# Kernel tuning notes

Measured on AMD Instinct MI355X. Metric: run time of the kernel, lower is better.

Reference implementation:

```python
import jax, jax.numpy as jnp
import numpy as np

WINDOW_SIZE = 11
SIGMA = 1.5
COLOR_TRANS = np.array([65.738, 129.057, 25.064], dtype=np.float32)
C1 = (0.01 * 255) ** 2
C2 = (0.03 * 255) ** 2


def _make_window(ws=WINDOW_SIZE, sigma=SIGMA):
    x = np.arange(ws, dtype=np.float32)
    g = np.exp(-((x - ws // 2) ** 2) / (2.0 * sigma ** 2))
    g = g / g.sum()
    w2d = np.outer(g, g).astype(np.float32)  # [ws, ws]
    return jnp.asarray(w2d[None, None])      # [1,1,ws,ws] OIHW


def _conv(x, w):
    # x: [B,1,H,W], w: [1,1,ws,ws], VALID padding, single channel
    return jax.lax.conv_general_dilated(
        x, w, window_strides=(1, 1), padding='VALID',
        dimension_numbers=('NCHW', 'OIHW', 'NCHW'))


def _luma(img):
    # img: [B,H,W,>=3] in [-1,1] -> [B,1,H,W] luma in [16,235]-ish
    rgb = (img[..., :3] + 1.0) / 2.0 * 255.0
    y = jnp.matmul(rgb, jnp.asarray(COLOR_TRANS)) / 256.0 + 16.0
    return y[:, None, :, :]


def setup_inputs() -> dict:
    key = jax.random.key(0)
    k1, k2 = jax.random.split(key)
    shape = (32, 512, 512, 3)
    img1 = jax.random.uniform(k1, shape, jnp.float32, -1.0, 1.0)
    img2 = jax.random.uniform(k2, shape, jnp.float32, -1.0, 1.0)
    return {"img1": img1, "img2": img2}


def reference(img1, img2):
    w = _make_window()
    x1 = _luma(img1)
    x2 = _luma(img2)
    mu1 = _conv(x1, w)
    mu2 = _conv(x2, w)
    mu1_sq = mu1 * mu1
    mu2_sq = mu2 * mu2
    mu1_mu2 = mu1 * mu2
    sigma1_sq = _conv(x1 * x1, w) - mu1_sq
    sigma2_sq = _conv(x2 * x2, w) - mu2_sq
    sigma12 = _conv(x1 * x2, w) - mu1_mu2
    ssim_map = ((2 * mu1_mu2 + C1) * (2 * sigma12 + C2)) / (
        (mu1_sq + mu2_sq + C1) * (sigma1_sq + sigma2_sq + C2))
    return jnp.mean(ssim_map)
```

## Files before the change

### kernel.cpp

```cpp
#include <hip/hip_runtime.h>
#include <math.h>

#define BATCH 32
#define H 512
#define W 512
#define OUTD 502
#define WS 11
#define STRIP 32
#define INROWS 42
#define WPAD 80

#define C1F 6.5025f
#define C2F 58.5225f
#define N_OUT_TOTAL 8064128.0

struct GW { float g[WS]; };

__device__ __forceinline__ float luma3(float r, float g, float b) {
    r = (r + 1.f) * 127.5f; g = (g + 1.f) * 127.5f; b = (b + 1.f) * 127.5f;
    return (r * 65.738f + g * 129.057f + b * 25.064f) * (1.f / 256.f) + 16.f;
}

__global__ __launch_bounds__(256) void ssim_stream_kernel(
    const float* __restrict__ img1, const float* __restrict__ img2,
    double* __restrict__ acc_out, GW wv)
{
    __shared__ float sbuf[2][4][2][WPAD];
    __shared__ double wsum[4];

    const int t    = threadIdx.x;
    const int lane = t & 63;
    const int wvid = t >> 6;
    const int cw = blockIdx.x * 256 + wvid * 64;
    const int ox = cw + lane;
    const int r0 = blockIdx.y * STRIP;
    const int b  = blockIdx.z;

    const bool colok = (ox < OUTD);
    const bool halo  = (lane < 10) && ((cw + 64 + lane) < W);
    const size_t imgbase = (size_t)b * (H * W * 3) + (size_t)r0 * (W * 3);
    const int colA = (cw + lane) * 3;
    const int colB = (cw + 64 + lane) * 3;

    float cA0, cA1, cA2, cB0, cB1, cB2, cC0, cC1, cC2, cD0, cD1, cD2;
    float nA0, nA1, nA2, nB0, nB1, nB2, nC0, nC1, nC2, nD0, nD1, nD2;

#define LOAD_RAW(IY, A0,A1,A2, B0,B1,B2, C0,C1v,C2v, D0,D1,D2)            \
    {                                                                     \
        A0=A1=A2=B0=B1=B2=C0=C1v=C2v=D0=D1=D2 = 0.f;                      \
        if ((IY) < INROWS && (r0 + (IY)) < H) {                           \
            const float* _q1 = img1 + imgbase + (size_t)((IY) * (W * 3)); \
            const float* _q2 = img2 + imgbase + (size_t)((IY) * (W * 3)); \
            A0 = _q1[colA]; A1 = _q1[colA + 1]; A2 = _q1[colA + 2];       \
            B0 = _q2[colA]; B1 = _q2[colA + 1]; B2 = _q2[colA + 2];       \
            if (halo) {                                                   \
                C0  = _q1[colB]; C1v = _q1[colB + 1]; C2v = _q1[colB + 2];\
                D0  = _q2[colB]; D1  = _q2[colB + 1]; D2  = _q2[colB + 2];\
            }                                                             \
        }                                                                 \
    }

#define STORE_ROW(IY)                                                     \
    {                                                                     \
        const int _p = (IY) & 1;                                          \
        sbuf[_p][wvid][0][lane] = luma3(cA0, cA1, cA2);                   \
        sbuf[_p][wvid][1][lane] = luma3(cB0, cB1, cB2);                   \
        if (lane < 10) {                                                  \
            sbuf[_p][wvid][0][64 + lane] = luma3(cC0, cC1, cC2);          \
            sbuf[_p][wvid][1][64 + lane] = luma3(cD0, cD1, cD2);          \
        }                                                                 \
    }

#define ROTATE_RAW()                                                      \
    {                                                                     \
        cA0 = nA0; cA1 = nA1; cA2 = nA2; cB0 = nB0; cB1 = nB1; cB2 = nB2; \
        cC0 = nC0; cC1 = nC1; cC2 = nC2; cD0 = nD0; cD1 = nD1; cD2 = nD2; \
    }

#define ROW_STEP(IY, H0, H1, H2, H3)                                      \
    {                                                                     \
        LOAD_RAW((IY) + 2, nA0,nA1,nA2, nB0,nB1,nB2,                      \
                           nC0,nC1,nC2, nD0,nD1,nD2);                     \
        STORE_ROW((IY) + 1);                                              \
        ROTATE_RAW();                                                     \
        {                                                                 \
            const int _rb = (IY) & 1;                                     \
            float _h0 = 0.f, _h1 = 0.f, _h2 = 0.f, _h3 = 0.f;             \
            _Pragma("unroll")                                             \
            for (int _k = 0; _k < WS; ++_k) {                             \
                const float _gk = wv.g[_k];                               \
                const float _a = sbuf[_rb][wvid][0][lane + _k];           \
                const float _c = sbuf[_rb][wvid][1][lane + _k];           \
                _h0 += _gk * _a;                                          \
                _h1 += _gk * _c;                                          \
                _h2 += _gk * (_a * _a + _c * _c);                         \
                _h3 += _gk * (_a * _c);                                   \
            }                                                             \
            H0 = _h0; H1 = _h1; H2 = _h2; H3 = _h3;                       \
        }                                                                 \
    }

    float rm1[WS], rm2[WS], rq[WS], rx[WS];
    #pragma unroll
    for (int s = 0; s < WS; ++s) {
        rm1[s] = 0.f; rm2[s] = 0.f; rq[s] = 0.f; rx[s] = 0.f;
    }

    LOAD_RAW(0, cA0,cA1,cA2, cB0,cB1,cB2, cC0,cC1,cC2, cD0,cD1,cD2);
    LOAD_RAW(1, nA0,nA1,nA2, nB0,nB1,nB2, nC0,nC1,nC2, nD0,nD1,nD2);
    STORE_ROW(0);
    ROTATE_RAW();

    #pragma unroll
    for (int j = 0; j < 10; ++j)
        ROW_STEP(j, rm1[j], rm2[j], rq[j], rx[j]);

    double local = 0.0;

#define DO_ROW(OY, JM)                                                    \
    {                                                                     \
        ROW_STEP((OY) + 10,                                               \
                 rm1[((JM) + 10) % WS], rm2[((JM) + 10) % WS],            \
                 rq[((JM) + 10) % WS],  rx[((JM) + 10) % WS]);            \
        float _mu1 = 0.f, _mu2 = 0.f, _eq = 0.f, _ex = 0.f;               \
        _Pragma("unroll")                                                 \
        for (int _k = 0; _k < WS; ++_k) {                                 \
            const float _gk = wv.g[_k];                                   \
            const int _s = ((JM) + _k) % WS;                              \
            _mu1 += _gk * rm1[_s];                                        \
            _mu2 += _gk * rm2[_s];                                        \
            _eq  += _gk * rq[_s];                                         \
            _ex  += _gk * rx[_s];                                         \
        }                                                                 \
        if (colok && (r0 + (OY)) < OUTD) {                                \
            const float _m1s = _mu1 * _mu1;                               \
            const float _m2s = _mu2 * _mu2;                               \
            const float _m12 = _mu1 * _mu2;                               \
            const float _num = (2.f * _m12 + C1F) *                       \
                               (2.f * (_ex - _m12) + C2F);                \
            const float _den = (_m1s + _m2s + C1F) *                      \
                               ((_eq - _m1s - _m2s) + C2F);               \
            local += (double)(_num / _den);                               \
        }                                                                 \
    }

    #pragma unroll 1
    for (int c = 0; c < 2; ++c) {
        const int base = c * 11;
        #pragma unroll
        for (int j = 0; j < 11; ++j)
            DO_ROW(base + j, j);
    }
    #pragma unroll
    for (int j = 0; j < 10; ++j)
        DO_ROW(22 + j, j);

    for (int off = 32; off > 0; off >>= 1)
        local += __shfl_down(local, off, 64);
    if (lane == 0) wsum[wvid] = local;
    __syncthreads();
    if (t == 0) {
        const double s = wsum[0] + wsum[1] + wsum[2] + wsum[3];
        atomicAdd(acc_out, s);
    }
}

__global__ void ssim_finalize_kernel(const double* __restrict__ acc,
                                     float* __restrict__ out)
{
    out[0] = (float)(acc[0] / N_OUT_TOTAL);
}

extern "C" void kernel_launch(void* const* d_in, const int* in_sizes, int n_in,
                              void* d_out, int out_size, void* d_ws, size_t ws_size,
                              hipStream_t stream) {
    const float* img1 = (const float*)d_in[0];
    const float* img2 = (const float*)d_in[1];
    float* out = (float*)d_out;
    double* acc = (double*)d_ws;

    GW w;
    {
        float g[WS];
        float s = 0.f;
        for (int i = 0; i < WS; ++i) {
            const float x = (float)(i - WS / 2);
            g[i] = expf(-(x * x) / (2.f * 1.5f * 1.5f));
            s += g[i];
        }
        for (int i = 0; i < WS; ++i) w.g[i] = g[i] / s;
    }

    hipMemsetAsync(d_ws, 0, sizeof(double), stream);

    dim3 grid(2, (OUTD + STRIP - 1) / STRIP, BATCH);
    ssim_stream_kernel<<<grid, 256, 0, stream>>>(img1, img2, acc, w);
    ssim_finalize_kernel<<<1, 1, 0, stream>>>(acc, out);
}
```

Before: 258.4 us.

## Precompute luma products into float4 LDS, use fast rcp and float accumulation

Each staged pixel now writes a float4 of (a, c, a²+c², a·c) to shared memory, so the horizontal pass does one vector LDS read per tap instead of two scalar reads plus redundant multiplies. Luma is folded into three FMAs with precombined constants, and the three-float pixel loads are grouped as one struct. The per-thread SSIM sum uses float with a hardware reciprocal instead of double and a true division, and the outer row loop is fully unrolled. The trade-off is slightly lower accuracy from rcp and float accumulation, plus higher LDS footprint and code size.

New measurement: 320.1 us. 1.24x slower.

```diff
diff --git a/kernel.cpp b/kernel.cpp
--- a/kernel.cpp
+++ b/kernel.cpp
@@ -15,17 +15,26 @@
 #define N_OUT_TOTAL 8064128.0
 
 struct GW { float g[WS]; };
+struct F3 { float x, y, z; };
+
+
+#define LDS_FENCE() asm volatile("" ::: "memory")
 
 __device__ __forceinline__ float luma3(float r, float g, float b) {
-    r = (r + 1.f) * 127.5f; g = (g + 1.f) * 127.5f; b = (b + 1.f) * 127.5f;
-    return (r * 65.738f + g * 129.057f + b * 25.064f) * (1.f / 256.f) + 16.f;
+    constexpr float W0 = 127.5f * 65.738f  / 256.f;
+    constexpr float W1 = 127.5f * 129.057f / 256.f;
+    constexpr float W2 = 127.5f * 25.064f  / 256.f;
+    constexpr float K0 = 127.5f * 65.738f  / 256.f
+                       + 127.5f * 129.057f / 256.f
+                       + 127.5f * 25.064f  / 256.f + 16.f;
+    return fmaf(r, W0, fmaf(g, W1, fmaf(b, W2, K0)));
 }
 
 __global__ __launch_bounds__(256) void ssim_stream_kernel(
     const float* __restrict__ img1, const float* __restrict__ img2,
     double* __restrict__ acc_out, GW wv)
 {
-    __shared__ float sbuf[2][4][2][WPAD];
+    __shared__ float4 sbuf[2][4][WPAD];
     __shared__ double wsum[4];
 
     const int t    = threadIdx.x;
@@ -51,11 +60,15 @@
         if ((IY) < INROWS && (r0 + (IY)) < H) {                           \
             const float* _q1 = img1 + imgbase + (size_t)((IY) * (W * 3)); \
             const float* _q2 = img2 + imgbase + (size_t)((IY) * (W * 3)); \
-            A0 = _q1[colA]; A1 = _q1[colA + 1]; A2 = _q1[colA + 2];       \
-            B0 = _q2[colA]; B1 = _q2[colA + 1]; B2 = _q2[colA + 2];       \
+            const F3 _pa = *reinterpret_cast<const F3*>(_q1 + colA);      \
+            const F3 _pb = *reinterpret_cast<const F3*>(_q2 + colA);      \
+            A0 = _pa.x; A1 = _pa.y; A2 = _pa.z;                           \
+            B0 = _pb.x; B1 = _pb.y; B2 = _pb.z;                           \
             if (halo) {                                                   \
-                C0  = _q1[colB]; C1v = _q1[colB + 1]; C2v = _q1[colB + 2];\
-                D0  = _q2[colB]; D1  = _q2[colB + 1]; D2  = _q2[colB + 2];\
+                const F3 _pc = *reinterpret_cast<const F3*>(_q1 + colB);  \
+                const F3 _pd = *reinterpret_cast<const F3*>(_q2 + colB);  \
+                C0  = _pc.x; C1v = _pc.y; C2v = _pc.z;                    \
+                D0  = _pd.x; D1  = _pd.y; D2  = _pd.z;                    \
             }                                                             \
         }                                                                 \
     }
@@ -63,12 +76,20 @@
 #define STORE_ROW(IY)                                                     \
     {                                                                     \
         const int _p = (IY) & 1;                                          \
-        sbuf[_p][wvid][0][lane] = luma3(cA0, cA1, cA2);                   \
-        sbuf[_p][wvid][1][lane] = luma3(cB0, cB1, cB2);                   \
+        LDS_FENCE();                                                      \
+        {                                                                 \
+            const float _a = luma3(cA0, cA1, cA2);                        \
+            const float _c = luma3(cB0, cB1, cB2);                        \
+            sbuf[_p][wvid][lane] =                                        \
+                make_float4(_a, _c, fmaf(_a, _a, _c * _c), _a * _c);      \
+        }                                                                 \
         if (lane < 10) {                                                  \
-            sbuf[_p][wvid][0][64 + lane] = luma3(cC0, cC1, cC2);          \
-            sbuf[_p][wvid][1][64 + lane] = luma3(cD0, cD1, cD2);          \
-        }                                                                 \
+            const float _a = luma3(cC0, cC1, cC2);                        \
+            const float _c = luma3(cD0, cD1, cD2);                        \
+            sbuf[_p][wvid][64 + lane] =                                   \
+                make_float4(_a, _c, fmaf(_a, _a, _c * _c), _a * _c);      \
+        }                                                                 \
+        LDS_FENCE();                                                      \
     }
 
 #define ROTATE_RAW()                                                      \
@@ -89,12 +110,11 @@
             _Pragma("unroll")                                             \
             for (int _k = 0; _k < WS; ++_k) {                             \
                 const float _gk = wv.g[_k];                               \
-                const float _a = sbuf[_rb][wvid][0][lane + _k];           \
-                const float _c = sbuf[_rb][wvid][1][lane + _k];           \
-                _h0 += _gk * _a;                                          \
-                _h1 += _gk * _c;                                          \
-                _h2 += _gk * (_a * _a + _c * _c);                         \
-                _h3 += _gk * (_a * _c);                                   \
+                const float4 _v = sbuf[_rb][wvid][lane + _k];             \
+                _h0 = fmaf(_gk, _v.x, _h0);                               \
+                _h1 = fmaf(_gk, _v.y, _h1);                               \
+                _h2 = fmaf(_gk, _v.z, _h2);                               \
+                _h3 = fmaf(_gk, _v.w, _h3);                               \
             }                                                             \
             H0 = _h0; H1 = _h1; H2 = _h2; H3 = _h3;                       \
         }                                                                 \
@@ -115,7 +135,7 @@
     for (int j = 0; j < 10; ++j)
         ROW_STEP(j, rm1[j], rm2[j], rq[j], rx[j]);
 
-    double local = 0.0;
+    float local = 0.f;
 
 #define DO_ROW(OY, JM)                                                    \
     {                                                                     \
@@ -127,10 +147,10 @@
         for (int _k = 0; _k < WS; ++_k) {                                 \
             const float _gk = wv.g[_k];                                   \
             const int _s = ((JM) + _k) % WS;                              \
-            _mu1 += _gk * rm1[_s];                                        \
-            _mu2 += _gk * rm2[_s];                                        \
-            _eq  += _gk * rq[_s];                                         \
-            _ex  += _gk * rx[_s];                                         \
+            _mu1 = fmaf(_gk, rm1[_s], _mu1);                              \
+            _mu2 = fmaf(_gk, rm2[_s], _mu2);                              \
+            _eq  = fmaf(_gk, rq[_s],  _eq);                               \
+            _ex  = fmaf(_gk, rx[_s],  _ex);                               \
         }                                                                 \
         if (colok && (r0 + (OY)) < OUTD) {                                \
             const float _m1s = _mu1 * _mu1;                               \
@@ -140,24 +160,23 @@
                                (2.f * (_ex - _m12) + C2F);                \
             const float _den = (_m1s + _m2s + C1F) *                      \
                                ((_eq - _m1s - _m2s) + C2F);               \
-            local += (double)(_num / _den);                               \
-        }                                                                 \
-    }
-
-    #pragma unroll 1
-    for (int c = 0; c < 2; ++c) {
-        const int base = c * 11;
-        #pragma unroll
-        for (int j = 0; j < 11; ++j)
-            DO_ROW(base + j, j);
-    }
+            local = fmaf(_num, __builtin_amdgcn_rcpf(_den), local);       \
+        }                                                                 \
+    }
+
+    #pragma unroll
+    for (int j = 0; j < 11; ++j)
+        DO_ROW(j, j);
+    #pragma unroll
+    for (int j = 0; j < 11; ++j)
+        DO_ROW(11 + j, j);
     #pragma unroll
     for (int j = 0; j < 10; ++j)
         DO_ROW(22 + j, j);
 
     for (int off = 32; off > 0; off >>= 1)
         local += __shfl_down(local, off, 64);
-    if (lane == 0) wsum[wvid] = local;
+    if (lane == 0) wsum[wvid] = (double)local;
     __syncthreads();
     if (t == 0) {
         const double s = wsum[0] + wsum[1] + wsum[2] + wsum[3];
```
